# Optimization experiments

Hardware: AMD Instinct MI355X
Metric: run time of the kernel (lower is better)

## Reference

```python
import jax, jax.numpy as jnp
import numpy as np

FACTOR = 2
FIR = (1.0, 3.0, 3.0, 1.0)  # resample_kernel from fir_kernel=(1,3,3,1)


def _fir_kernel_2d(dtype):
    # StyleGAN2 _setup_kernel: outer product, normalize, then * gain * factor^2
    k = np.asarray(FIR, dtype=np.float64)
    k = np.outer(k, k)
    k /= k.sum()
    k *= FACTOR ** 2
    return jnp.asarray(k, dtype)


def setup_inputs() -> dict:
    key = jax.random.key(0)
    kx, kw, kb = jax.random.split(key, 3)
    B, H, W, C, O = 16, 64, 64, 128, 128
    x = jax.random.normal(kx, (B, H, W, C), jnp.float32)
    fan_avg = (3 * 3 * C + 3 * 3 * O) / 2.0  # default_init ~ variance_scaling fan_avg
    w = jax.random.normal(kw, (3, 3, C, O), jnp.float32) * np.float32(np.sqrt(1.0 / fan_avg))
    b = jax.random.normal(kb, (O,), jnp.float32) * 0.1
    return {"x": x, "w": w, "b": b}


def reference(x, w, b):
    B, H, W, C = x.shape
    kh = w.shape[0]  # 3
    # Step 1: stride-2 transposed conv, VALID. tf.nn.conv2d_transpose with the
    # double-flipped/transposed weights reduces exactly to plain correlation of
    # the zero-dilated input with w (HWIO).  -> (B, 2H+1, 2W+1, O)
    y = jax.lax.conv_general_dilated(
        x, w,
        window_strides=(1, 1),
        padding=((kh - 1, kh - 1), (kh - 1, kh - 1)),
        lhs_dilation=(FACTOR, FACTOR),
        dimension_numbers=('NHWC', 'HWIO', 'NHWC'))
    # Step 2: depthwise FIR filtering (upfirdn2d with up=down=1 and the fused pads)
    k2d = _fir_kernel_2d(x.dtype)
    kwid = k2d.shape[0]  # 4
    p = (kwid - FACTOR) - (kh - 1)          # = 0
    pad0 = (p + 1) // 2 + FACTOR - 1        # = 1
    pad1 = p // 2 + 1                       # = 1
    O = y.shape[-1]
    # upfirdn uses true convolution -> flip kernel (symmetric here, but faithful)
    fir = jnp.tile(k2d[::-1, ::-1][:, :, None, None], (1, 1, 1, O))
    y = jax.lax.conv_general_dilated(
        y, fir,
        window_strides=(1, 1),
        padding=((pad0, pad1), (pad0, pad1)),
        dimension_numbers=('NHWC', 'HWIO', 'NHWC'),
        feature_group_count=O)              # (B, 2H, 2W, O)
    return y + b.reshape(1, 1, 1, -1)
```

## Files before the change

### kernel.cpp

```cpp
#include <hip/hip_runtime.h>
#include <hip/hip_bf16.h>

#define BB 16
#define HH 64
#define WW 64
#define CC 128
#define OO 128

typedef __attribute__((ext_vector_type(8))) short bf16x8;
typedef __attribute__((ext_vector_type(4))) float f32x4;

__constant__ float Kc[2][3][3] = {
    {{0.75f, 0.25f, 0.00f}, {0.25f, 0.75f, 0.75f}, {0.00f, 0.00f, 0.25f}},
    {{0.25f, 0.00f, 0.00f}, {0.75f, 0.75f, 0.25f}, {0.00f, 0.25f, 0.75f}},
};

__device__ __forceinline__ unsigned short f2bf(float f) {
    union { float f; unsigned u; } a; a.f = f;
    unsigned r = a.u + 0x7fffu + ((a.u >> 16) & 1u);
    return (unsigned short)(r >> 16);
}

__global__ void pack_b_kernel(const float* __restrict__ w, unsigned short* __restrict__ bp) {
    int l  = threadIdx.x;
    int nf = blockIdx.x;
    int ks = blockIdx.y;
    int ph = blockIdx.z;
    int ps = ph >> 1, pt = ph & 1;
    int o = nf * 16 + (l & 15);
    int chunk = l >> 4;
    size_t off = ((((size_t)ph * 36 + ks) * 8 + nf) * 64 + l) * 8;
    for (int j = 0; j < 8; ++j) {
        int k = ks * 32 + chunk * 8 + j;
        int didj = k >> 7;
        int c = k & 127;
        int di = didj / 3, dj = didj % 3;
        float acc = 0.f;
        for (int a = 0; a < 3; ++a) {
            float ka = Kc[ps][di][a];
            for (int bq = 0; bq < 3; ++bq) {
                acc += ka * Kc[pt][dj][bq] * w[((a * 3 + bq) * CC + c) * OO + o];
            }
        }
        bp[off + j] = f2bf(acc);
    }
}

__launch_bounds__(256, 2)
__global__ void upconv_kernel(const float* __restrict__ x,
                              const unsigned short* __restrict__ bp,
                              const float* __restrict__ bias,
                              float* __restrict__ out) {
    __shared__ unsigned short xs[6 * 18 * 128];

    const int tid = threadIdx.x;
    const int gT0 = blockIdx.x * 16;
    const int gS0 = blockIdx.y * 4;
    const int b   = blockIdx.z;

    for (int i = tid; i < 6 * 18 * 16; i += 256) {
        int c8  = i & 15;
        int rc  = i >> 4;
        int col = rc % 18;
        int r   = rc / 18;
        int gr = gS0 - 1 + r;
        int gc = gT0 - 1 + col;
        float4 v0 = make_float4(0.f, 0.f, 0.f, 0.f);
        float4 v1 = v0;
        if ((unsigned)gr < HH && (unsigned)gc < WW) {
            const float* p = x + (((size_t)b * HH + gr) * WW + gc) * CC + c8 * 8;
            v0 = *(const float4*)p;
            v1 = *(const float4*)(p + 4);
        }
        unsigned short tmp[8];
        tmp[0] = f2bf(v0.x); tmp[1] = f2bf(v0.y); tmp[2] = f2bf(v0.z); tmp[3] = f2bf(v0.w);
        tmp[4] = f2bf(v1.x); tmp[5] = f2bf(v1.y); tmp[6] = f2bf(v1.z); tmp[7] = f2bf(v1.w);
        int byte = (((r * 18 + col) * 128 + c8 * 8) * 2) ^ ((col & 7) << 4);
        *(bf16x8*)((char*)xs + byte) = *(const bf16x8*)tmp;
    }
    __syncthreads();

    const int wid    = tid >> 6;
    const int l      = tid & 63;
    const int lane15 = l & 15;
    const int chunk  = l >> 4;
    const int ps = wid >> 1, pt = wid & 1;

    f32x4 acc[4][8];
    #pragma unroll
    for (int mi = 0; mi < 4; ++mi)
        #pragma unroll
        for (int ni = 0; ni < 8; ++ni)
            acc[mi][ni] = (f32x4){0.f, 0.f, 0.f, 0.f};

    const bf16x8* bpv = (const bf16x8*)bp + (size_t)wid * 36 * 8 * 64;

    for (int ks = 0; ks < 36; ++ks) {
        int didj = ks >> 2;
        int di = didj / 3, dj = didj % 3;
        int c0 = (ks & 3) * 32 + chunk * 8;
        bf16x8 af[4];
        #pragma unroll
        for (int mi = 0; mi < 4; ++mi) {
            int r   = mi + di;
            int col = lane15 + dj;
            int byte = (((r * 18 + col) * 128 + c0) * 2) ^ ((col & 7) << 4);
            af[mi] = *(const bf16x8*)((const char*)xs + byte);
        }
        const bf16x8* bkv = bpv + (size_t)ks * 8 * 64 + l;
        #pragma unroll
        for (int ni = 0; ni < 8; ++ni) {
            bf16x8 bfv = bkv[ni * 64];
            #pragma unroll
            for (int mi = 0; mi < 4; ++mi)
                acc[mi][ni] = __builtin_amdgcn_mfma_f32_16x16x32_bf16(af[mi], bfv, acc[mi][ni], 0, 0, 0);
        }
    }

    #pragma unroll
    for (int ni = 0; ni < 8; ++ni) {
        int o = ni * 16 + lane15;
        float bv = bias[o];
        #pragma unroll
        for (int mi = 0; mi < 4; ++mi) {
            int s = 2 * (gS0 + mi) + ps;
            #pragma unroll
            for (int rg = 0; rg < 4; ++rg) {
                int t = 2 * (gT0 + chunk * 4 + rg) + pt;
                out[(((size_t)b * 128 + s) * 128 + t) * 128 + o] = acc[mi][ni][rg] + bv;
            }
        }
    }
}

extern "C" void kernel_launch(void* const* d_in, const int* in_sizes, int n_in,
                              void* d_out, int out_size, void* d_ws, size_t ws_size,
                              hipStream_t stream) {
    const float* x    = (const float*)d_in[0];
    const float* w    = (const float*)d_in[1];
    const float* bias = (const float*)d_in[2];
    float* out        = (float*)d_out;
    unsigned short* bp = (unsigned short*)d_ws;

    dim3 gp(8, 36, 4);
    pack_b_kernel<<<gp, 64, 0, stream>>>(w, bp);

    dim3 gm(4, 16, 16);
    upconv_kernel<<<gm, 256, 0, stream>>>(x, bp, bias, out);
}
```

Baseline: 241.7 us.

## Software-pipeline B fragment loads, hoist FIR weights in pack, nontemporal output stores

The main GEMM loop now splits the B fragments into two halves and prefetches the first half of the next k-step while the MFMAs for the current step run, aiming to hide global load latency behind matrix math. The pack kernel hoists the combined FIR tap products out of the per-element loop and unrolls it. Output stores become nontemporal to avoid polluting cache with the large write stream. The extra prefetch registers may raise register pressure under the two-blocks-per-CU launch bound.

```diff
diff --git a/kernel.cpp b/kernel.cpp
--- a/kernel.cpp
+++ b/kernel.cpp
@@ -27,21 +27,28 @@
     int ks = blockIdx.y;
     int ph = blockIdx.z;
     int ps = ph >> 1, pt = ph & 1;
+    int didj = ks >> 2;
+    int di = didj / 3, dj = didj % 3;
+    float kk[3][3];
+    #pragma unroll
+    for (int a = 0; a < 3; ++a)
+        #pragma unroll
+        for (int bq = 0; bq < 3; ++bq)
+            kk[a][bq] = Kc[ps][di][a] * Kc[pt][dj][bq];
+
     int o = nf * 16 + (l & 15);
     int chunk = l >> 4;
+    int cbase = (ks & 3) * 32 + chunk * 8;
     size_t off = ((((size_t)ph * 36 + ks) * 8 + nf) * 64 + l) * 8;
+    #pragma unroll
     for (int j = 0; j < 8; ++j) {
-        int k = ks * 32 + chunk * 8 + j;
-        int didj = k >> 7;
-        int c = k & 127;
-        int di = didj / 3, dj = didj % 3;
+        int c = cbase + j;
         float acc = 0.f;
-        for (int a = 0; a < 3; ++a) {
-            float ka = Kc[ps][di][a];
-            for (int bq = 0; bq < 3; ++bq) {
-                acc += ka * Kc[pt][dj][bq] * w[((a * 3 + bq) * CC + c) * OO + o];
-            }
-        }
+        #pragma unroll
+        for (int a = 0; a < 3; ++a)
+            #pragma unroll
+            for (int bq = 0; bq < 3; ++bq)
+                acc += kk[a][bq] * w[((a * 3 + bq) * CC + c) * OO + o];
         bp[off + j] = f2bf(acc);
     }
 }
@@ -95,7 +102,20 @@
 
     const bf16x8* bpv = (const bf16x8*)bp + (size_t)wid * 36 * 8 * 64;
 
+    bf16x8 b0[4];
+    {
+        const bf16x8* bk = bpv + l;
+        #pragma unroll
+        for (int ni = 0; ni < 4; ++ni) b0[ni] = bk[ni * 64];
+    }
+
+    #pragma unroll 4
     for (int ks = 0; ks < 36; ++ks) {
+        const bf16x8* bk = bpv + (size_t)ks * 512 + l;
+        bf16x8 b1[4];
+        #pragma unroll
+        for (int ni = 0; ni < 4; ++ni) b1[ni] = bk[(ni + 4) * 64];
+
         int didj = ks >> 2;
         int di = didj / 3, dj = didj % 3;
         int c0 = (ks & 3) * 32 + chunk * 8;
@@ -107,14 +127,28 @@
             int byte = (((r * 18 + col) * 128 + c0) * 2) ^ ((col & 7) << 4);
             af[mi] = *(const bf16x8*)((const char*)xs + byte);
         }
-        const bf16x8* bkv = bpv + (size_t)ks * 8 * 64 + l;
+
         #pragma unroll
-        for (int ni = 0; ni < 8; ++ni) {
-            bf16x8 bfv = bkv[ni * 64];
+        for (int ni = 0; ni < 4; ++ni)
             #pragma unroll
             for (int mi = 0; mi < 4; ++mi)
-                acc[mi][ni] = __builtin_amdgcn_mfma_f32_16x16x32_bf16(af[mi], bfv, acc[mi][ni], 0, 0, 0);
+                acc[mi][ni] = __builtin_amdgcn_mfma_f32_16x16x32_bf16(af[mi], b0[ni], acc[mi][ni], 0, 0, 0);
+
+        bf16x8 bn[4];
+        if (ks + 1 < 36) {
+            const bf16x8* bk2 = bpv + (size_t)(ks + 1) * 512 + l;
+            #pragma unroll
+            for (int ni = 0; ni < 4; ++ni) bn[ni] = bk2[ni * 64];
         }
+
+        #pragma unroll
+        for (int ni = 0; ni < 4; ++ni)
+            #pragma unroll
+            for (int mi = 0; mi < 4; ++mi)
+                acc[mi][ni + 4] = __builtin_amdgcn_mfma_f32_16x16x32_bf16(af[mi], b1[ni], acc[mi][ni + 4], 0, 0, 0);
+
+        #pragma unroll
+        for (int ni = 0; ni < 4; ++ni) b0[ni] = bn[ni];
     }
 
     #pragma unroll
@@ -127,7 +161,8 @@
             #pragma unroll
             for (int rg = 0; rg < 4; ++rg) {
                 int t = 2 * (gT0 + chunk * 4 + rg) + pt;
-                out[(((size_t)b * 128 + s) * 128 + t) * 128 + o] = acc[mi][ni][rg] + bv;
+                __builtin_nontemporal_store(acc[mi][ni][rg] + bv,
+                    &out[(((size_t)b * 128 + s) * 128 + t) * 128 + o]);
             }
         }
     }
```

New measurement: 237.7 us. About the same (-1.7%).
